# Kernel optimization log

Hardware: AMD Instinct MI355X
Metric: run time of the kernel (lower is better)

## Reference

```python
import jax, jax.numpy as jnp
import numpy as np

NEG_INF = -1.0e10  # matches -10000000000.0 in the original


def setup_inputs() -> dict:
    key0 = jax.random.key(0)
    kq, kk, kv = jax.random.split(key0, 3)
    b, t, n, n_kv, d = 1, 2048, 32, 8, 128
    query = jax.random.normal(kq, (b, t, n, d), dtype=jnp.float32)
    key = jax.random.normal(kk, (b, t, n_kv, d), dtype=jnp.float32)
    value = jax.random.normal(kv, (b, t, n_kv, d), dtype=jnp.float32)
    return {"query": query, "key": key, "value": value}


def reference(query, key, value):
    """PagedAttentionOp prefill path: paged_dot_product_attention_with_max_and_sum.

    Returns (attn, local_max, local_sums) exactly as the flax module does.
    """
    b, t, n, d = query.shape
    _, s, n_kv, _ = key.shape
    g = n // n_kv  # query heads per KV head (GQA group size)
    q = jnp.reshape(query, (b, t, n_kv, g, d))
    # [b, n_kv, g, t, s]
    attn_weights = jnp.einsum("btkgd,bskd->bkgts", q, key)
    causal_mask = jnp.triu(jnp.ones((t, s), dtype=bool), k=1)[None, None, None]
    masked = jnp.where(causal_mask, NEG_INF, attn_weights)
    local_max = jnp.max(masked, axis=-1, keepdims=True)          # [b,k,g,t,1]
    local_exps = jnp.exp(masked - local_max)
    local_sums = jnp.sum(local_exps, axis=-1, keepdims=True)     # [b,k,g,t,1]
    attn = jnp.einsum("bkgts,bskd->btkgd", local_exps, value)
    attn = jnp.reshape(attn, (b, t, n, d))
    # move the t axis to position 1 then flatten (k,g) -> n
    local_max = jnp.reshape(jnp.moveaxis(local_max, -2, 1), (b, t, n, 1))
    local_sums = jnp.reshape(jnp.moveaxis(local_sums, -2, 1), (b, t, n, 1))
    return attn, local_max, local_sums
```

## Files before the change

kernel.cpp:

```cpp
#include <hip/hip_runtime.h>
#include <hip/hip_bf16.h>

#define TT  2048
#define NH  32
#define NKV 8
#define DD  128
#define KVB 64

typedef __attribute__((ext_vector_type(8)))  short  short8;
typedef __attribute__((ext_vector_type(4)))  float  f32x4;
typedef __attribute__((ext_vector_type(16))) float  f32x16;
typedef unsigned int u32;
typedef __attribute__((ext_vector_type(4)))  u32    u32x4;

static __device__ __forceinline__ short f2bf(float x) {
  __bf16 b = (__bf16)x;
  return __builtin_bit_cast(short, b);
}
static __device__ __forceinline__ short8 cvt8(f32x4 a, f32x4 b) {
  short8 r;
  r[0]=f2bf(a[0]); r[1]=f2bf(a[1]); r[2]=f2bf(a[2]); r[3]=f2bf(a[3]);
  r[4]=f2bf(b[0]); r[5]=f2bf(b[1]); r[6]=f2bf(b[2]); r[7]=f2bf(b[3]);
  return r;
}
static __device__ __forceinline__ u32 pk2(float lo, float hi) {
  const u32 a = (u32)(unsigned short)f2bf(lo);
  const u32 b = (u32)(unsigned short)f2bf(hi);
  return a | (b << 16);
}
static __device__ __forceinline__ void gload_lds16(const short* g, short* l) {
  __builtin_amdgcn_global_load_lds(
      (const __attribute__((address_space(1))) u32*)g,
      (__attribute__((address_space(3))) u32*)l, 16, 0, 0);
}

__global__ __launch_bounds__(256) void preconv(
    const float* __restrict__ K, const float* __restrict__ V,
    short* __restrict__ Kbf, short* __restrict__ Vtbf)
{
  const int t = threadIdx.x;
  if (blockIdx.x >= 256) {
    const int b  = blockIdx.x - 256;
    const int rr = (b << 6) + (t >> 2);
    const int q  = t & 3;
    const int j = rr >> 3, kvh = rr & 7;
    const float* src = K + (size_t)rr * DD + q * 32;
    short* dst = Kbf + ((size_t)kvh * TT + j) * DD + q * 32;
#pragma unroll
    for (int i = 0; i < 4; ++i) {
      f32x4 a  = *reinterpret_cast<const f32x4*>(src + i * 8);
      f32x4 bb = *reinterpret_cast<const f32x4*>(src + i * 8 + 4);
      *reinterpret_cast<short8*>(dst + i * 8) = cvt8(a, bb);
    }
  } else {
    const int kvh = blockIdx.x >> 5, jt = blockIdx.x & 31;
    __shared__ short Vl[64][136];
    const int jl = t >> 2, q = t & 3;
    const float* src = V + ((size_t)(jt * 64 + jl) * NKV + kvh) * DD + q * 32;
#pragma unroll
    for (int i = 0; i < 4; ++i) {
      f32x4 a  = *reinterpret_cast<const f32x4*>(src + i * 8);
      f32x4 bb = *reinterpret_cast<const f32x4*>(src + i * 8 + 4);
      *reinterpret_cast<short8*>(&Vl[jl][q * 32 + i * 8]) = cvt8(a, bb);
    }
    __syncthreads();
    const int d = t >> 1, jh = t & 1;
    short8 o[4];
#pragma unroll
    for (int k = 0; k < 4; ++k)
#pragma unroll
      for (int i = 0; i < 8; ++i)
        o[k][i] = Vl[jh * 32 + k * 8 + i][d];
    short* dst = Vtbf + ((size_t)kvh * DD + d) * TT + jt * 64 + jh * 32;
#pragma unroll
    for (int k = 0; k < 4; ++k)
      *reinterpret_cast<short8*>(dst + k * 8) = o[k];
  }
}

__global__ __launch_bounds__(256, 2) void attn_fwd(
    const float* __restrict__ Q, const short* __restrict__ Kbf,
    const short* __restrict__ Vtbf, float* __restrict__ O,
    float* __restrict__ Mo, float* __restrict__ Lo)
{
  __shared__ __align__(16) short Kb[2][KVB][DD];
  __shared__ __align__(16) short Vt[2][DD][KVB];

  const int bid  = blockIdx.x;
  const int kvh  = bid & (NKV - 1);
  const int jj   = bid >> 3;
  const int q32  = (jj < 32) ? (63 - jj) : (jj - 32);
  const int wv   = threadIdx.x >> 6;
  const int lane = threadIdx.x & 63;
  const int l31  = lane & 31;
  const int hiK  = lane >> 5;
  const int l7   = lane & 7;
  const int head = kvh * 4 + wv;
  const int qbase = q32 * 32;
  const int q    = qbase + l31;

  int koff[4];
#pragma unroll
  for (int t = 0; t < 4; ++t) {
    const int row = 16 * wv + 4 * t + (lane >> 4);
    const int ch  = (lane & 15) ^ (4 * (t & 1) + (lane >> 4));
    koff[t] = row * DD + ch * 8;
  }
  const int vrow0 = 32 * wv + (lane >> 3);
  const int vch   = (lane & 7) ^ (lane >> 3);
  const int voffB = vrow0 * TT + vch * 8;

  short8 aq[8];
  {
    const float* qp = Q + ((size_t)q * NH + head) * DD + hiK * 8;
#pragma unroll
    for (int ks = 0; ks < 8; ++ks) {
      const float* p = qp + ks * 16;
      aq[ks] = cvt8(*reinterpret_cast<const f32x4*>(p),
                    *reinterpret_cast<const f32x4*>(p + 4));
    }
  }

  f32x16 acc[4];
#pragma unroll
  for (int i = 0; i < 4; ++i) acc[i] = (f32x16)0.0f;
  float m = -INFINITY, lsum = 0.0f;

  const int ntiles = (q32 >> 1) + 1;

  const short* kgp = Kbf + (size_t)kvh * TT * DD;
  const short* vgp = Vtbf + (size_t)kvh * DD * TT;

#pragma unroll
  for (int t = 0; t < 4; ++t)
    gload_lds16(kgp + koff[t], &Kb[0][16 * wv + 4 * t][0]);
#pragma unroll
  for (int t = 0; t < 4; ++t)
    gload_lds16(vgp + voffB + t * 8 * TT, &Vt[0][32 * wv + 8 * t][0]);
  kgp += (size_t)KVB * DD;
  vgp += KVB;

  for (int jt = 0; jt < ntiles; ++jt) {
    const int j0  = jt << 6;
    const int buf = jt & 1;

    __syncthreads();

    if (jt + 1 < ntiles) {
      const int nb = buf ^ 1;
#pragma unroll
      for (int t = 0; t < 4; ++t)
        gload_lds16(kgp + koff[t], &Kb[nb][16 * wv + 4 * t][0]);
#pragma unroll
      for (int t = 0; t < 4; ++t)
        gload_lds16(vgp + voffB + t * 8 * TT, &Vt[nb][32 * wv + 8 * t][0]);
      kgp += (size_t)KVB * DD;
      vgp += KVB;
    }

    f32x16 st[2];
    st[0] = (f32x16)0.0f; st[1] = (f32x16)0.0f;
    __builtin_amdgcn_s_setprio(1);
#pragma unroll
    for (int kg = 0; kg < 2; ++kg) {
      const short* kr = &Kb[buf][kg * 32 + l31][0];
#pragma unroll
      for (int ks = 0; ks < 8; ++ks) {
        const int c = ((ks << 1) | hiK) ^ l7;
        short8 kb = *reinterpret_cast<const short8*>(kr + c * 8);
        st[kg] = __builtin_amdgcn_mfma_f32_32x32x16_bf16(kb, aq[ks], st[kg], 0, 0, 0);
      }
    }
    __builtin_amdgcn_s_setprio(0);

    if (jt == ntiles - 1) {
#pragma unroll
      for (int kg = 0; kg < 2; ++kg)
#pragma unroll
        for (int r = 0; r < 16; ++r) {
          const int key = j0 + kg * 32 + (r & 3) + 8 * (r >> 2) + 4 * hiK;
          if (key > q) st[kg][r] = -1.0e10f;
        }
    }

    float mx = fmaxf(st[0][0], st[1][0]);
#pragma unroll
    for (int r = 1; r < 16; ++r) mx = fmaxf(mx, fmaxf(st[0][r], st[1][r]));
    mx = fmaxf(mx, __shfl_xor(mx, 32, 64));

    if (__any(mx > m)) {
      const float mn = fmaxf(m, mx);
      const float sc = __expf(m - mn);
      m = mn;
      lsum *= sc;
#pragma unroll
      for (int r = 0; r < 16; ++r) {
        const float sf = __shfl(sc, (r & 3) + 8 * (r >> 2) + 4 * hiK, 64);
        acc[0][r] *= sf; acc[1][r] *= sf; acc[2][r] *= sf; acc[3][r] *= sf;
      }
    }

    short8 pa[4];
#pragma unroll
    for (int kg = 0; kg < 2; ++kg) {
      float e[16];
#pragma unroll
      for (int r = 0; r < 16; ++r) e[r] = __expf(st[kg][r] - m);
      lsum += (((e[0]+e[1])+(e[2]+e[3]))+((e[4]+e[5])+(e[6]+e[7])))
            + (((e[8]+e[9])+(e[10]+e[11]))+((e[12]+e[13])+(e[14]+e[15])));
#pragma unroll
      for (int h2 = 0; h2 < 2; ++h2) {
        const int b = 8 * h2;
        u32 u0 = pk2(e[b+0], e[b+1]);
        u32 u1 = pk2(e[b+2], e[b+3]);
        u32 u2 = pk2(e[b+4], e[b+5]);
        u32 u3 = pk2(e[b+6], e[b+7]);
        u32 sA = hiK ? u0 : u2;
        u32 sB = hiK ? u1 : u3;
        u32 rA = __shfl_xor(sA, 32, 64);
        u32 rB = __shfl_xor(sB, 32, 64);
        u32x4 w;
        w[0] = hiK ? rA : u0;
        w[1] = hiK ? rB : u1;
        w[2] = hiK ? u2 : rA;
        w[3] = hiK ? u3 : rB;
        pa[kg * 2 + h2] = __builtin_bit_cast(short8, w);
      }
    }

    __builtin_amdgcn_s_setprio(1);
#pragma unroll
    for (int dg = 0; dg < 4; ++dg) {
      const short* vr = &Vt[buf][dg * 32 + l31][0];
#pragma unroll
      for (int ks = 0; ks < 4; ++ks) {
        const int c = ((ks << 1) | hiK) ^ l7;
        short8 vb = *reinterpret_cast<const short8*>(vr + c * 8);
        acc[dg] = __builtin_amdgcn_mfma_f32_32x32x16_bf16(pa[ks], vb, acc[dg], 0, 0, 0);
      }
    }
    __builtin_amdgcn_s_setprio(0);
  }

  const float lsumT = lsum + __shfl_xor(lsum, 32, 64);

#pragma unroll
  for (int r = 0; r < 16; ++r) {
    const int row = (r & 3) + 8 * (r >> 2) + 4 * hiK;
    const size_t ob = ((size_t)(qbase + row) * NH + head) * DD + l31;
#pragma unroll
    for (int dg = 0; dg < 4; ++dg)
      O[ob + dg * 32] = acc[dg][r];
  }

  if (lane < 32) {
    Mo[(size_t)q * NH + head] = m;
    Lo[(size_t)q * NH + head] = lsumT;
  }
}

extern "C" void kernel_launch(void* const* d_in, const int* in_sizes, int n_in,
                              void* d_out, int out_size, void* d_ws, size_t ws_size,
                              hipStream_t stream) {
  const float* Q = (const float*)d_in[0];
  const float* K = (const float*)d_in[1];
  const float* V = (const float*)d_in[2];
  float* O  = (float*)d_out;
  float* Mo = O + (size_t)TT * NH * DD;
  float* Lo = Mo + (size_t)TT * NH;
  short* Kbf  = (short*)d_ws;
  short* Vtbf = Kbf + (size_t)NKV * TT * DD;
  preconv<<<dim3(512), dim3(256), 0, stream>>>(K, V, Kbf, Vtbf);
  attn_fwd<<<dim3(64 * NKV), dim3(256), 0, stream>>>(Q, Kbf, Vtbf, O, Mo, Lo);
}
```

Before: 88.35 us.

## Split KV tile across two wave groups and merge partial softmax states

Result: faster. 81.44 us (-7.8%).

```diff
diff --git a/kernel.cpp b/kernel.cpp
--- a/kernel.cpp
+++ b/kernel.cpp
@@ -6,6 +6,7 @@
 #define NKV 8
 #define DD  128
 #define KVB 64
+#define THR 8.0f
 
 typedef __attribute__((ext_vector_type(8)))  short  short8;
 typedef __attribute__((ext_vector_type(4)))  float  f32x4;
@@ -78,37 +79,38 @@
   }
 }
 
-__global__ __launch_bounds__(256, 2) void attn_fwd(
+__global__ __launch_bounds__(512, 2) void attn_fwd(
     const float* __restrict__ Q, const short* __restrict__ Kbf,
     const short* __restrict__ Vtbf, float* __restrict__ O,
     float* __restrict__ Mo, float* __restrict__ Lo)
 {
-  __shared__ __align__(16) short Kb[2][KVB][DD];
-  __shared__ __align__(16) short Vt[2][DD][KVB];
+  __shared__ __align__(16) short smem[2*KVB*DD + 2*DD*KVB];
+  __shared__ float sx[3][2][4][32];
+
+  short (*Kb)[KVB][DD] = reinterpret_cast<short(*)[KVB][DD]>(&smem[0]);
+  short (*Vt)[DD][KVB] = reinterpret_cast<short(*)[DD][KVB]>(&smem[2*KVB*DD]);
 
   const int bid  = blockIdx.x;
   const int kvh  = bid & (NKV - 1);
-  const int jj   = bid >> 3;
-  const int q32  = (jj < 32) ? (63 - jj) : (jj - 32);
+  const int q32  = 63 - (bid >> 3);
   const int wv   = threadIdx.x >> 6;
+  const int headq= wv & 3;
+  const int kh   = wv >> 2;
   const int lane = threadIdx.x & 63;
   const int l31  = lane & 31;
   const int hiK  = lane >> 5;
   const int l7   = lane & 7;
-  const int head = kvh * 4 + wv;
+  const int head = kvh * 4 + headq;
   const int qbase = q32 * 32;
   const int q    = qbase + l31;
 
-  int koff[4];
-#pragma unroll
-  for (int t = 0; t < 4; ++t) {
-    const int row = 16 * wv + 4 * t + (lane >> 4);
-    const int ch  = (lane & 15) ^ (4 * (t & 1) + (lane >> 4));
-    koff[t] = row * DD + ch * 8;
-  }
-  const int vrow0 = 32 * wv + (lane >> 3);
-  const int vch   = (lane & 7) ^ (lane >> 3);
-  const int voffB = vrow0 * TT + vch * 8;
+  const int krow0 = 8 * wv + (lane >> 4);
+  const int koff0 = krow0 * DD + ((lane & 15) ^ (krow0 & 7)) * 8;
+  const int krow1 = krow0 + 4;
+  const int koff1 = krow1 * DD + ((lane & 15) ^ (krow1 & 7)) * 8;
+  const int vrow0 = 16 * wv + (lane >> 3);
+  const int voff0 = vrow0 * TT + ((lane & 7) ^ (lane >> 3)) * 8;
+  const int voff1 = voff0 + 8 * TT;
 
   short8 aq[8];
   {
@@ -124,19 +126,17 @@
   f32x16 acc[4];
 #pragma unroll
   for (int i = 0; i < 4; ++i) acc[i] = (f32x16)0.0f;
-  float m = -INFINITY, lsum = 0.0f;
+  float m = -INFINITY, tmaxh = -INFINITY, lsum = 0.0f;
 
   const int ntiles = (q32 >> 1) + 1;
 
   const short* kgp = Kbf + (size_t)kvh * TT * DD;
   const short* vgp = Vtbf + (size_t)kvh * DD * TT;
 
-#pragma unroll
-  for (int t = 0; t < 4; ++t)
-    gload_lds16(kgp + koff[t], &Kb[0][16 * wv + 4 * t][0]);
-#pragma unroll
-  for (int t = 0; t < 4; ++t)
-    gload_lds16(vgp + voffB + t * 8 * TT, &Vt[0][32 * wv + 8 * t][0]);
+  gload_lds16(kgp + koff0, &Kb[0][8 * wv][0]);
+  gload_lds16(kgp + koff1, &Kb[0][8 * wv + 4][0]);
+  gload_lds16(vgp + voff0, &Vt[0][16 * wv][0]);
+  gload_lds16(vgp + voff1, &Vt[0][16 * wv + 8][0]);
   kgp += (size_t)KVB * DD;
   vgp += KVB;
 
@@ -146,49 +146,42 @@
 
     __syncthreads();
 
+    f32x16 st = (f32x16)0.0f;
+    const short* kr = &Kb[buf][kh * 32 + l31][0];
+    __builtin_amdgcn_s_setprio(1);
+#pragma unroll
+    for (int ks = 0; ks < 8; ++ks) {
+      const int c = ((ks << 1) | hiK) ^ l7;
+      short8 kb = *reinterpret_cast<const short8*>(kr + c * 8);
+      st = __builtin_amdgcn_mfma_f32_32x32x16_bf16(kb, aq[ks], st, 0, 0, 0);
+    }
+    __builtin_amdgcn_s_setprio(0);
+
     if (jt + 1 < ntiles) {
       const int nb = buf ^ 1;
-#pragma unroll
-      for (int t = 0; t < 4; ++t)
-        gload_lds16(kgp + koff[t], &Kb[nb][16 * wv + 4 * t][0]);
-#pragma unroll
-      for (int t = 0; t < 4; ++t)
-        gload_lds16(vgp + voffB + t * 8 * TT, &Vt[nb][32 * wv + 8 * t][0]);
+      gload_lds16(kgp + koff0, &Kb[nb][8 * wv][0]);
+      gload_lds16(kgp + koff1, &Kb[nb][8 * wv + 4][0]);
+      gload_lds16(vgp + voff0, &Vt[nb][16 * wv][0]);
+      gload_lds16(vgp + voff1, &Vt[nb][16 * wv + 8][0]);
       kgp += (size_t)KVB * DD;
       vgp += KVB;
     }
 
-    f32x16 st[2];
-    st[0] = (f32x16)0.0f; st[1] = (f32x16)0.0f;
-    __builtin_amdgcn_s_setprio(1);
-#pragma unroll
-    for (int kg = 0; kg < 2; ++kg) {
-      const short* kr = &Kb[buf][kg * 32 + l31][0];
-#pragma unroll
-      for (int ks = 0; ks < 8; ++ks) {
-        const int c = ((ks << 1) | hiK) ^ l7;
-        short8 kb = *reinterpret_cast<const short8*>(kr + c * 8);
-        st[kg] = __builtin_amdgcn_mfma_f32_32x32x16_bf16(kb, aq[ks], st[kg], 0, 0, 0);
+    if (jt == ntiles - 1) {
+#pragma unroll
+      for (int r = 0; r < 16; ++r) {
+        const int key = j0 + kh * 32 + (r & 3) + 8 * (r >> 2) + 4 * hiK;
+        if (key > q) st[r] = -1.0e10f;
       }
     }
-    __builtin_amdgcn_s_setprio(0);
-
-    if (jt == ntiles - 1) {
-#pragma unroll
-      for (int kg = 0; kg < 2; ++kg)
-#pragma unroll
-        for (int r = 0; r < 16; ++r) {
-          const int key = j0 + kg * 32 + (r & 3) + 8 * (r >> 2) + 4 * hiK;
-          if (key > q) st[kg][r] = -1.0e10f;
-        }
-    }
-
-    float mx = fmaxf(st[0][0], st[1][0]);
-#pragma unroll
-    for (int r = 1; r < 16; ++r) mx = fmaxf(mx, fmaxf(st[0][r], st[1][r]));
+
+    float mx = st[0];
+#pragma unroll
+    for (int r = 1; r < 16; ++r) mx = fmaxf(mx, st[r]);
     mx = fmaxf(mx, __shfl_xor(mx, 32, 64));
-
-    if (__any(mx > m)) {
+    tmaxh = fmaxf(tmaxh, mx);
+
+    if (__any(mx > m + THR)) {
       const float mn = fmaxf(m, mx);
       const float sc = __expf(m - mn);
       m = mn;
@@ -200,32 +193,30 @@
       }
     }
 
-    short8 pa[4];
-#pragma unroll
-    for (int kg = 0; kg < 2; ++kg) {
-      float e[16];
-#pragma unroll
-      for (int r = 0; r < 16; ++r) e[r] = __expf(st[kg][r] - m);
-      lsum += (((e[0]+e[1])+(e[2]+e[3]))+((e[4]+e[5])+(e[6]+e[7])))
-            + (((e[8]+e[9])+(e[10]+e[11]))+((e[12]+e[13])+(e[14]+e[15])));
-#pragma unroll
-      for (int h2 = 0; h2 < 2; ++h2) {
-        const int b = 8 * h2;
-        u32 u0 = pk2(e[b+0], e[b+1]);
-        u32 u1 = pk2(e[b+2], e[b+3]);
-        u32 u2 = pk2(e[b+4], e[b+5]);
-        u32 u3 = pk2(e[b+6], e[b+7]);
-        u32 sA = hiK ? u0 : u2;
-        u32 sB = hiK ? u1 : u3;
-        u32 rA = __shfl_xor(sA, 32, 64);
-        u32 rB = __shfl_xor(sB, 32, 64);
-        u32x4 w;
-        w[0] = hiK ? rA : u0;
-        w[1] = hiK ? rB : u1;
-        w[2] = hiK ? u2 : rA;
-        w[3] = hiK ? u3 : rB;
-        pa[kg * 2 + h2] = __builtin_bit_cast(short8, w);
-      }
+    float e[16];
+#pragma unroll
+    for (int r = 0; r < 16; ++r) e[r] = __expf(st[r] - m);
+    lsum += (((e[0]+e[1])+(e[2]+e[3]))+((e[4]+e[5])+(e[6]+e[7])))
+          + (((e[8]+e[9])+(e[10]+e[11]))+((e[12]+e[13])+(e[14]+e[15])));
+
+    short8 pa[2];
+#pragma unroll
+    for (int h2 = 0; h2 < 2; ++h2) {
+      const int b = 8 * h2;
+      u32 u0 = pk2(e[b+0], e[b+1]);
+      u32 u1 = pk2(e[b+2], e[b+3]);
+      u32 u2 = pk2(e[b+4], e[b+5]);
+      u32 u3 = pk2(e[b+6], e[b+7]);
+      u32 sA = hiK ? u0 : u2;
+      u32 sB = hiK ? u1 : u3;
+      u32 rA = __shfl_xor(sA, 32, 64);
+      u32 rB = __shfl_xor(sB, 32, 64);
+      u32x4 w;
+      w[0] = hiK ? rA : u0;
+      w[1] = hiK ? rB : u1;
+      w[2] = hiK ? u2 : rA;
+      w[3] = hiK ? u3 : rB;
+      pa[h2] = __builtin_bit_cast(short8, w);
     }
 
     __builtin_amdgcn_s_setprio(1);
@@ -233,29 +224,57 @@
     for (int dg = 0; dg < 4; ++dg) {
       const short* vr = &Vt[buf][dg * 32 + l31][0];
 #pragma unroll
-      for (int ks = 0; ks < 4; ++ks) {
-        const int c = ((ks << 1) | hiK) ^ l7;
+      for (int h2 = 0; h2 < 2; ++h2) {
+        const int ksv = 2 * kh + h2;
+        const int c = ((ksv << 1) | hiK) ^ l7;
         short8 vb = *reinterpret_cast<const short8*>(vr + c * 8);
-        acc[dg] = __builtin_amdgcn_mfma_f32_32x32x16_bf16(pa[ks], vb, acc[dg], 0, 0, 0);
+        acc[dg] = __builtin_amdgcn_mfma_f32_32x32x16_bf16(pa[h2], vb, acc[dg], 0, 0, 0);
       }
     }
     __builtin_amdgcn_s_setprio(0);
   }
 
-  const float lsumT = lsum + __shfl_xor(lsum, 32, 64);
-
-#pragma unroll
-  for (int r = 0; r < 16; ++r) {
-    const int row = (r & 3) + 8 * (r >> 2) + 4 * hiK;
-    const size_t ob = ((size_t)(qbase + row) * NH + head) * DD + l31;
-#pragma unroll
-    for (int dg = 0; dg < 4; ++dg)
-      O[ob + dg * 32] = acc[dg][r];
-  }
-
+  const float lw = lsum + __shfl_xor(lsum, 32, 64);
+  __syncthreads();
   if (lane < 32) {
-    Mo[(size_t)q * NH + head] = m;
-    Lo[(size_t)q * NH + head] = lsumT;
+    sx[0][kh][headq][lane] = m;
+    sx[1][kh][headq][lane] = tmaxh;
+    sx[2][kh][headq][lane] = lw;
+  }
+  __syncthreads();
+  const float mo   = sx[0][kh ^ 1][headq][l31];
+  const float to   = sx[1][kh ^ 1][headq][l31];
+  const float lo2  = sx[2][kh ^ 1][headq][l31];
+  const float tmax = fmaxf(tmaxh, to);
+  const float fsA  = __expf(m - tmax);
+  const float ltot = lw * fsA + lo2 * __expf(mo - tmax);
+
+  float* mbuf = reinterpret_cast<float*>(&smem[0]);
+  if (kh == 1) {
+#pragma unroll
+    for (int r = 0; r < 16; ++r) {
+      const int row = (r & 3) + 8 * (r >> 2) + 4 * hiK;
+      const float sfr = __shfl(fsA, row, 64);
+#pragma unroll
+      for (int dg = 0; dg < 4; ++dg)
+        mbuf[headq * 4096 + row * 128 + dg * 32 + l31] = acc[dg][r] * sfr;
+    }
+  }
+  __syncthreads();
+  if (kh == 0) {
+#pragma unroll
+    for (int r = 0; r < 16; ++r) {
+      const int row = (r & 3) + 8 * (r >> 2) + 4 * hiK;
+      const float sfr = __shfl(fsA, row, 64);
+      const size_t ob = ((size_t)(qbase + row) * NH + head) * DD + l31;
+#pragma unroll
+      for (int dg = 0; dg < 4; ++dg)
+        O[ob + dg * 32] = acc[dg][r] * sfr + mbuf[headq * 4096 + row * 128 + dg * 32 + l31];
+    }
+    if (lane < 32) {
+      Mo[(size_t)q * NH + head] = tmax;
+      Lo[(size_t)q * NH + head] = ltot;
+    }
   }
 }
 
@@ -271,5 +290,5 @@
   short* Kbf  = (short*)d_ws;
   short* Vtbf = Kbf + (size_t)NKV * TT * DD;
   preconv<<<dim3(512), dim3(256), 0, stream>>>(K, V, Kbf, Vtbf);
-  attn_fwd<<<dim3(64 * NKV), dim3(256), 0, stream>>>(Q, Kbf, Vtbf, O, Mo, Lo);
-}
+  attn_fwd<<<dim3(64 * NKV), dim3(512), 0, stream>>>(Q, Kbf, Vtbf, O, Mo, Lo);
+}
```
